# Performance work log

Hardware: AMD Instinct MI355X
Metric: run time of the kernel (lower is better)

The kernel has to match this reference:

```python
import jax, jax.numpy as jnp
import numpy as np

N_NODES = 100000


def setup_inputs() -> dict:
    key = jax.random.key(0)
    k1, k2, k3 = jax.random.split(key, 3)
    X = jax.random.normal(k1, (N_NODES, 128), dtype=jnp.float32)
    W = jax.random.normal(k2, (128, 128), dtype=jnp.float32) * (1.0 / np.sqrt(128))
    edge_index = jax.random.randint(k3, (2, 1600000), 0, N_NODES, dtype=jnp.int64)
    return {"X": X, "W": W, "edge_index": edge_index}


def reference(X, W, edge_index):
    # GCNConv: out = D_hat^{-1/2} (A + I) D_hat^{-1/2} @ (X W^T)
    N = X.shape[0]
    row, col = edge_index[0], edge_index[1]
    # A_hat = A + I : append self-loop edges
    loops = jnp.arange(N, dtype=row.dtype)
    row_h = jnp.concatenate([row, loops])
    col_h = jnp.concatenate([col, loops])
    # D_hat = A_hat.sum(0): column sums -> degree indexed by col
    deg = jax.ops.segment_sum(jnp.ones(col_h.shape[0], dtype=X.dtype), col_h,
                              num_segments=N)
    d_invsqrt = deg ** -0.5  # deg >= 1 due to self loops
    # edge value of H = D^-1/2 A_hat D^-1/2
    val = d_invsqrt[row_h] * d_invsqrt[col_h]  # [E+N]
    # linear projection (nn.Linear, no bias): X @ W^T
    X_hat = X @ W.T  # [N, out]
    # SpMM (sum): out[r] += val * X_hat[c]
    msgs = val[:, None] * X_hat[col_h]  # [E+N, out]
    return jax.ops.segment_sum(msgs, row_h, num_segments=N)
```

## Files before the change

kernel.cpp:

```cpp
#include <hip/hip_runtime.h>
#include <hip/hip_bf16.h>
#include <stdint.h>

typedef __bf16 bf16_t;
typedef bf16_t bf16x8 __attribute__((ext_vector_type(8)));
typedef bf16_t bf16x2 __attribute__((ext_vector_type(2)));
typedef float  f32x4  __attribute__((ext_vector_type(4)));
typedef float  f32x2  __attribute__((ext_vector_type(2)));

#define N_FEAT 128
#define NBMAX  196
#define BINB   512

__global__ void detect_k(const int* __restrict__ edges, int* __restrict__ flag) {
    int v = edges[2 * threadIdx.x + 1];
    unsigned long long m = __ballot(v != 0);
    if (threadIdx.x == 0) *flag = (m == 0ull) ? 1 : 0;
}
__device__ inline int eread(const int* __restrict__ edges, int f, long i) {
    return f ? edges[2 * i] : edges[i];
}

__device__ inline bf16x8 cvt8(const float* __restrict__ p) {
    f32x4 lo = *(const f32x4*)p;
    f32x4 hi = *(const f32x4*)(p + 4);
    bf16x8 r;
    r[0] = (bf16_t)lo[0]; r[1] = (bf16_t)lo[1]; r[2] = (bf16_t)lo[2]; r[3] = (bf16_t)lo[3];
    r[4] = (bf16_t)hi[0]; r[5] = (bf16_t)hi[1]; r[6] = (bf16_t)hi[2]; r[7] = (bf16_t)hi[3];
    return r;
}

__device__ inline int block_scan_incl(int v, int* wsum ) {
    const int t = threadIdx.x, lane = t & 63, wid = t >> 6;
    int x = v;
#pragma unroll
    for (int off = 1; off < 64; off <<= 1) {
        int y = __shfl_up(x, off);
        if (lane >= off) x += y;
    }
    if (lane == 63) wsum[wid] = x;
    __syncthreads();
    int add = 0;
    for (int w = 0; w < wid; ++w) add += wsum[w];
    return x + add;
}

__global__ __launch_bounds__(256) void wconv_k(const float* __restrict__ W,
                                               bf16_t* __restrict__ Wbf) {
    int i = blockIdx.x * 256 + threadIdx.x;
    Wbf[i] = (bf16_t)W[i];
}

__global__ __launch_bounds__(64) void gemm_xwt2(const float* __restrict__ X,
                                                const bf16_t* __restrict__ Wbf,
                                                bf16_t* __restrict__ Xhat) {
    const int lane = threadIdx.x;
    const int m  = lane & 15;
    const int kq = lane >> 4;
    const long r0 = (long)blockIdx.x * 16;

    f32x4 acc[8];
#pragma unroll
    for (int c = 0; c < 8; ++c) acc[c] = (f32x4){0.f, 0.f, 0.f, 0.f};

    const float* xrow = X + (r0 + m) * N_FEAT + kq * 8;
#pragma unroll
    for (int kb = 0; kb < 4; ++kb) {
        bf16x8 a = cvt8(xrow + kb * 32);
#pragma unroll
        for (int c = 0; c < 8; ++c) {
            bf16x8 b = *(const bf16x8*)(Wbf + (c * 16 + m) * N_FEAT + kb * 32 + kq * 8);
            acc[c] = __builtin_amdgcn_mfma_f32_16x16x32_bf16(a, b, acc[c], 0, 0, 0);
        }
    }
#pragma unroll
    for (int c = 0; c < 8; ++c) {
#pragma unroll
        for (int i = 0; i < 4; ++i) {
            long r = r0 + kq * 4 + i;
            Xhat[r * N_FEAT + c * 16 + m] = (bf16_t)acc[c][i];
        }
    }
}


__global__ __launch_bounds__(256) void bin_k(const int* __restrict__ edges,
                                             const int* __restrict__ flag,
                                             int E, int N, int NB,
                                             int* __restrict__ hist) {
    __shared__ int h[2 * NBMAX];
    const int blk = blockIdx.x;
    const int nb2 = 2 * NB;
    for (int j = threadIdx.x; j < nb2; j += 256) h[j] = 0;
    __syncthreads();
    const int f = *flag;
    const int chunk = (E + BINB - 1) / BINB;
    const int e0 = blk * chunk, e1 = min(E, e0 + chunk);
    if (f) {
        const int2* e2 = (const int2*)edges;
        for (int e = e0 + (int)threadIdx.x; e < e1; e += 256) {
            int r = e2[e].x, c = e2[(long)E + e].x;
            if ((unsigned)r < (unsigned)N && (unsigned)c < (unsigned)N) {
                atomicAdd(&h[r >> 9], 1);
                atomicAdd(&h[NB + (c >> 9)], 1);
            }
        }
    } else {
        for (int e = e0 + (int)threadIdx.x; e < e1; e += 256) {
            int r = edges[e], c = edges[(long)E + e];
            if ((unsigned)r < (unsigned)N && (unsigned)c < (unsigned)N) {
                atomicAdd(&h[r >> 9], 1);
                atomicAdd(&h[NB + (c >> 9)], 1);
            }
        }
    }
    __syncthreads();
    for (int j = threadIdx.x; j < nb2; j += 256) hist[(long)j * BINB + blk] = h[j];
}

__global__ __launch_bounds__(BINB) void scan_k(const int* __restrict__ hist, int NB,
                                               int* __restrict__ baseTab,
                                               int* __restrict__ totals) {
    __shared__ int wsum[BINB / 64];
    const int j = blockIdx.x;
    const int t = threadIdx.x;
    int v = hist[(long)j * BINB + t];
    int incl = block_scan_incl(v, wsum);
    baseTab[(long)j * BINB + t] = incl - v;
    if (t == BINB - 1) totals[j] = incl;
}

__global__ __launch_bounds__(512) void bucketbase_k(const int* __restrict__ totals,
                                                    int NB, int N,
                                                    int* __restrict__ famBase,
                                                    int* __restrict__ start) {
    __shared__ int wsum[8];
    __shared__ int sh_tot0;
    const int t = threadIdx.x;
    const int nb2 = 2 * NB;
    int v = (t < nb2) ? totals[t] : 0;
    int incl = block_scan_incl(v, wsum);
    int excl = incl - v;
    if (t == NB) sh_tot0 = excl;
    __syncthreads();
    if (t < NB) famBase[t] = excl;
    if (t == NB) { famBase[NB] = excl; start[N] = excl; }
    if (t >= NB && t < nb2) famBase[NB + 1 + (t - NB)] = excl - sh_tot0;
    if (t == nb2 - 1) famBase[NB + 1 + NB] = incl - sh_tot0;
}

__global__ __launch_bounds__(256) void bscatter_k(const int* __restrict__ edges,
                                                  const int* __restrict__ flag,
                                                  int E, int N, int NB,
                                                  const int* __restrict__ baseTab,
                                                  const int* __restrict__ famBase,
                                                  unsigned* __restrict__ rowbuf,
                                                  int* __restrict__ colbuf) {
    __shared__ int cur[2 * NBMAX];
    const int blk = blockIdx.x;
    const int nb2 = 2 * NB;
    for (int j = threadIdx.x; j < nb2; j += 256) {
        int fb = (j < NB) ? famBase[j] : famBase[NB + 1 + (j - NB)];
        cur[j] = fb + baseTab[(long)j * BINB + blk];
    }
    __syncthreads();
    const int f = *flag;
    const int chunk = (E + BINB - 1) / BINB;
    const int e0 = blk * chunk, e1 = min(E, e0 + chunk);
    if (f) {
        const int2* e2 = (const int2*)edges;
        for (int e = e0 + (int)threadIdx.x; e < e1; e += 256) {
            int r = e2[e].x, c = e2[(long)E + e].x;
            if ((unsigned)r < (unsigned)N && (unsigned)c < (unsigned)N) {
                int pr = atomicAdd(&cur[r >> 9], 1);
                rowbuf[pr] = ((unsigned)(r & 511) << 17) | (unsigned)c;
                int pc = atomicAdd(&cur[NB + (c >> 9)], 1);
                colbuf[pc] = c & 511;
            }
        }
    } else {
        for (int e = e0 + (int)threadIdx.x; e < e1; e += 256) {
            int r = edges[e], c = edges[(long)E + e];
            if ((unsigned)r < (unsigned)N && (unsigned)c < (unsigned)N) {
                int pr = atomicAdd(&cur[r >> 9], 1);
                rowbuf[pr] = ((unsigned)(r & 511) << 17) | (unsigned)c;
                int pc = atomicAdd(&cur[NB + (c >> 9)], 1);
                colbuf[pc] = c & 511;
            }
        }
    }
}

__global__ __launch_bounds__(512) void degcsr_k(const unsigned* __restrict__ rowbuf,
                                                const int* __restrict__ colbuf,
                                                const int* __restrict__ famBase,
                                                int NB, int N,
                                                int* __restrict__ start,
                                                int* __restrict__ ecol,
                                                float* __restrict__ dinv) {
    __shared__ int cnt[512];
    __shared__ int wsum[8];
    const int t = threadIdx.x;
    if ((int)blockIdx.x >= NB) {
        const int b = blockIdx.x - NB;
        cnt[t] = 0;
        __syncthreads();
        const int e0 = famBase[NB + 1 + b], e1 = famBase[NB + 1 + b + 1];
        for (int e = e0 + t; e < e1; e += 512)
            atomicAdd(&cnt[colbuf[e]], 1);
        __syncthreads();
        int n = (b << 9) + t;
        if (n < N) dinv[n] = rsqrtf((float)(cnt[t] + 1));
        return;
    }
    const int b = blockIdx.x;
    cnt[t] = 0;
    __syncthreads();
    const int e0 = famBase[b], e1 = famBase[b + 1];
    for (int e = e0 + t; e < e1; e += 512)
        atomicAdd(&cnt[rowbuf[e] >> 17], 1);
    __syncthreads();
    int v = cnt[t];
    int incl = block_scan_incl(v, wsum);
    int excl = incl - v;
    const int n = (b << 9) + t;
    if (n < N) start[n] = e0 + excl;
    cnt[t] = e0 + excl;
    __syncthreads();
    for (int e = e0 + t; e < e1; e += 512) {
        unsigned w = rowbuf[e];
        int pos = atomicAdd(&cnt[w >> 17], 1);
        ecol[pos] = (int)(w & 0x1FFFFu);
    }
}

__global__ __launch_bounds__(64) void gather3_k(const int* __restrict__ ecol,
                                                const int* __restrict__ start,
                                                const float* __restrict__ dinv,
                                                const bf16_t* __restrict__ Xhat,
                                                float* __restrict__ out) {
    const int n = blockIdx.x;
    const int j = threadIdx.x;
    const int s = start[n], e = start[n + 1];
    const float dn = dinv[n];

    bf16x2 xs = *(const bf16x2*)(Xhat + (long)n * N_FEAT + 2 * j);
    float a0 = dn * (float)xs[0];
    float a1 = dn * (float)xs[1];

    for (int p = s; p < e; p += 8) {
        int   cq[8];
        float dq[8];
#pragma unroll
        for (int q = 0; q < 8; ++q) {
            int tt = p + q;
            int idx = (tt < e) ? tt : s;
            cq[q] = ecol[idx];
            dq[q] = (tt < e) ? dinv[cq[q]] : 0.0f;
        }
#pragma unroll
        for (int q = 0; q < 8; ++q) {
            bf16x2 xv = *(const bf16x2*)(Xhat + (long)cq[q] * N_FEAT + 2 * j);
            a0 += dq[q] * (float)xv[0];
            a1 += dq[q] * (float)xv[1];
        }
    }
    f32x2 o; o[0] = dn * a0; o[1] = dn * a1;
    *(f32x2*)(out + (long)n * N_FEAT + 2 * j) = o;
}


__global__ __launch_bounds__(64) void gemm_xwt(const float* __restrict__ X,
                                               const float* __restrict__ W,
                                               bf16_t* __restrict__ Xhat) {
    const int lane = threadIdx.x;
    const int m  = lane & 15;
    const int kq = lane >> 4;
    const long r0 = (long)blockIdx.x * 16;
    f32x4 acc[8];
#pragma unroll
    for (int c = 0; c < 8; ++c) acc[c] = (f32x4){0.f, 0.f, 0.f, 0.f};
    const float* xrow = X + (r0 + m) * N_FEAT + kq * 8;
#pragma unroll
    for (int kb = 0; kb < 4; ++kb) {
        bf16x8 a = cvt8(xrow + kb * 32);
#pragma unroll
        for (int c = 0; c < 8; ++c) {
            bf16x8 b = cvt8(W + (c * 16 + m) * N_FEAT + kb * 32 + kq * 8);
            acc[c] = __builtin_amdgcn_mfma_f32_16x16x32_bf16(a, b, acc[c], 0, 0, 0);
        }
    }
#pragma unroll
    for (int c = 0; c < 8; ++c)
#pragma unroll
        for (int i = 0; i < 4; ++i) {
            long r = r0 + kq * 4 + i;
            Xhat[r * N_FEAT + c * 16 + m] = (bf16_t)acc[c][i];
        }
}

__global__ void degree_k(const int* __restrict__ edges, const int* __restrict__ flag,
                         int E, int N,
                         int* __restrict__ cnt_row, int* __restrict__ cnt_col) {
    int e = blockIdx.x * blockDim.x + threadIdx.x;
    int f = *flag;
    if (e < E) {
        int r = eread(edges, f, e);
        int c = eread(edges, f, (long)E + e);
        if ((unsigned)r < (unsigned)N) atomicAdd(&cnt_row[r], 1);
        if ((unsigned)c < (unsigned)N) atomicAdd(&cnt_col[c], 1);
    }
}

__global__ void degree_col_k(const int* __restrict__ edges, const int* __restrict__ flag,
                             int E, int N, int* __restrict__ cnt_col) {
    int e = blockIdx.x * blockDim.x + threadIdx.x;
    int f = *flag;
    if (e < E) {
        int c = eread(edges, f, (long)E + e);
        if ((unsigned)c < (unsigned)N) atomicAdd(&cnt_col[c], 1);
    }
}

__global__ void alloc_k(const int* __restrict__ cnt_row, int N,
                        int* __restrict__ cur, int* __restrict__ total,
                        int* cnt_col_in, float* dinv_out) {
    int n = blockIdx.x * blockDim.x + threadIdx.x;
    if (n < N) {
        cur[n] = atomicAdd(total, cnt_row[n]);
        int dc = cnt_col_in[n];
        dinv_out[n] = rsqrtf((float)(dc + 1));
    }
}

__global__ void scatter_k(const int* __restrict__ edges, const int* __restrict__ flag,
                          int E, int N, int* __restrict__ cur, int* __restrict__ ecol) {
    int e = blockIdx.x * blockDim.x + threadIdx.x;
    int f = *flag;
    if (e < E) {
        int r = eread(edges, f, e);
        if ((unsigned)r < (unsigned)N) {
            int p = atomicAdd(&cur[r], 1);
            if ((unsigned)p < (unsigned)E)
                ecol[p] = eread(edges, f, (long)E + e);
        }
    }
}

__global__ __launch_bounds__(64) void gather_k(const int* __restrict__ ecol,
                                               const int* __restrict__ cur,
                                               const int* __restrict__ cnt_row,
                                               const float* __restrict__ dinv,
                                               const bf16_t* __restrict__ Xhat,
                                               int N,
                                               float* __restrict__ out) {
    const int n = blockIdx.x;
    const int j = threadIdx.x;
    const int c = cnt_row[n];
    const int s = cur[n] - c;
    const float dn = dinv[n];
    bf16x2 xs = *(const bf16x2*)(Xhat + (long)n * N_FEAT + 2 * j);
    float a0 = dn * (float)xs[0];
    float a1 = dn * (float)xs[1];
    for (int e = 0; e < c; ++e) {
        int cc = ecol[s + e];
        if ((unsigned)cc >= (unsigned)N) continue;
        float dc = dinv[cc];
        bf16x2 xv = *(const bf16x2*)(Xhat + (long)cc * N_FEAT + 2 * j);
        a0 += dc * (float)xv[0];
        a1 += dc * (float)xv[1];
    }
    f32x2 o; o[0] = dn * a0; o[1] = dn * a1;
    *(f32x2*)(out + (long)n * N_FEAT + 2 * j) = o;
}


__global__ __launch_bounds__(128) void self_k(const int* __restrict__ cnt_col,
                                              const bf16_t* __restrict__ Xhat,
                                              float* __restrict__ out) {
    const int n = blockIdx.x;
    const int j = threadIdx.x;
    const float dn2 = 1.0f / (float)(cnt_col[n] + 1);
    out[(long)n * N_FEAT + j] = dn2 * (float)Xhat[(long)n * N_FEAT + j];
}

__global__ __launch_bounds__(128) void edge_add_k(const int* __restrict__ edges,
                                                  const int* __restrict__ flag,
                                                  int E, int N,
                                                  const int* __restrict__ cnt_col,
                                                  const bf16_t* __restrict__ Xhat,
                                                  float* __restrict__ out) {
    const int e = blockIdx.x;
    const int j = threadIdx.x;
    int f = *flag;
    const int r = eread(edges, f, e);
    const int c = eread(edges, f, (long)E + e);
    if ((unsigned)r >= (unsigned)N || (unsigned)c >= (unsigned)N) return;
    const float val = rsqrtf((float)(cnt_col[r] + 1)) * rsqrtf((float)(cnt_col[c] + 1));
    atomicAdd(&out[(long)r * N_FEAT + j], val * (float)Xhat[(long)c * N_FEAT + j]);
}

extern "C" void kernel_launch(void* const* d_in, const int* in_sizes, int n_in,
                              void* d_out, int out_size, void* d_ws, size_t ws_size,
                              hipStream_t stream) {
    const float* X = (const float*)d_in[0];
    const float* W = (const float*)d_in[1];
    const int* edges = (const int*)d_in[2];
    const int E = in_sizes[2] / 2;
    const int N = in_sizes[0] / N_FEAT;
    const int NB = (N + 511) >> 9;

    char* ws = (char*)d_ws;
    const size_t xhat_b = (size_t)N * N_FEAT * sizeof(bf16_t);
    const size_t n4     = (size_t)N * 4;
    auto al = [](size_t x) { return (x + 255) & ~(size_t)255; };

    size_t off = 0;
    int*      flag   = (int*)(ws + off);        off = 256;
    bf16_t*   Wbf    = (bf16_t*)(ws + off);     off = al(off + 128 * 128 * 2);
    bf16_t*   Xhat   = (bf16_t*)(ws + off);     off = al(off + xhat_b);
    float*    dinv   = (float*)(ws + off);      off = al(off + n4);
    int*      startA = (int*)(ws + off);        off = al(off + n4 + 4);
    unsigned* rowbuf = (unsigned*)(ws + off);   off = al(off + (size_t)E * 4);
    int*      colbuf = (int*)(ws + off);        off = al(off + (size_t)E * 4);
    int*      ecol   = (int*)(ws + off);        off = al(off + (size_t)E * 4);
    int*      hist   = (int*)(ws + off);        off = al(off + (size_t)BINB * 2 * NB * 4);
    int*      baseTab= (int*)(ws + off);        off = al(off + (size_t)BINB * 2 * NB * 4);
    int*      totals = (int*)(ws + off);        off = al(off + (size_t)(2 * NB) * 4);
    int*      famBase= (int*)(ws + off);        off = al(off + (size_t)(2 * NB + 2) * 4);
    const size_t need_S = off;

    int* cnt_col = (int*)(ws + 16 + xhat_b);
    const size_t need_A = 16 + xhat_b + n4 * 3 + 16 + (size_t)E * 4;
    const size_t need_B = 16 + xhat_b + n4;

    if (ws_size >= need_S && NB <= NBMAX && N <= 100352 && (N & 15) == 0 && E >= BINB) {
        detect_k<<<1, 64, 0, stream>>>(edges, flag);
        wconv_k<<<64, 256, 0, stream>>>(W, Wbf);
        gemm_xwt2<<<N / 16, 64, 0, stream>>>(X, Wbf, Xhat);
        bin_k<<<BINB, 256, 0, stream>>>(edges, flag, E, N, NB, hist);
        scan_k<<<2 * NB, BINB, 0, stream>>>(hist, NB, baseTab, totals);
        bucketbase_k<<<1, 512, 0, stream>>>(totals, NB, N, famBase, startA);
        bscatter_k<<<BINB, 256, 0, stream>>>(edges, flag, E, N, NB, baseTab, famBase,
                                             rowbuf, colbuf);
        degcsr_k<<<2 * NB, 512, 0, stream>>>(rowbuf, colbuf, famBase, NB, N,
                                             startA, ecol, dinv);
        gather3_k<<<N, 64, 0, stream>>>(ecol, startA, dinv, Xhat, (float*)d_out);
    } else if (ws_size >= need_A) {
        bf16_t* XhatA  = (bf16_t*)(ws + 16);
        int*   cnt_row = (int*)(ws + 16 + xhat_b + n4);
        int*   cur     = (int*)(ws + 16 + xhat_b + n4 * 2);
        int*   total   = (int*)(ws + 16 + xhat_b + n4 * 3);
        int*   ecolA   = (int*)(ws + 16 + xhat_b + n4 * 3 + 16);
        float* dinvA   = (float*)cnt_col;

        hipMemsetAsync(cnt_col, 0, n4 * 2, stream);
        hipMemsetAsync(total, 0, 16, stream);
        detect_k<<<1, 64, 0, stream>>>(edges, flag);
        gemm_xwt<<<N / 16, 64, 0, stream>>>(X, W, XhatA);
        degree_k<<<(E + 255) / 256, 256, 0, stream>>>(edges, flag, E, N, cnt_row, cnt_col);
        alloc_k<<<(N + 255) / 256, 256, 0, stream>>>(cnt_row, N, cur, total, cnt_col, dinvA);
        scatter_k<<<(E + 255) / 256, 256, 0, stream>>>(edges, flag, E, N, cur, ecolA);
        gather_k<<<N, 64, 0, stream>>>(ecolA, cur, cnt_row, dinvA, XhatA, N, (float*)d_out);
    } else if (ws_size >= need_B) {
        bf16_t* XhatB = (bf16_t*)(ws + 16);
        hipMemsetAsync(cnt_col, 0, n4, stream);
        detect_k<<<1, 64, 0, stream>>>(edges, flag);
        gemm_xwt<<<N / 16, 64, 0, stream>>>(X, W, XhatB);
        degree_col_k<<<(E + 255) / 256, 256, 0, stream>>>(edges, flag, E, N, cnt_col);
        self_k<<<N, 128, 0, stream>>>(cnt_col, XhatB, (float*)d_out);
        edge_add_k<<<E, 128, 0, stream>>>(edges, flag, E, N, cnt_col, XhatB, (float*)d_out);
    }
}
```

Before: 270.8 us.

## Prescale Xhat by dinv in GEMM and drop per-edge dinv gathers

The GEMM now runs after the degree computation and multiplies each output row by its inverse-sqrt degree before writing bf16 Xhat. The gather therefore skips the per-edge dinv lookup, sending padded lanes to a zero row appended to Xhat instead. The separate detect kernel is folded into bin_k and bscatter_k, which removes one launch. The cost is that the GEMM can no longer overlap the graph-build kernels in stream order, and pre-scaling before the bf16 rounding changes numerics slightly.

Measured after the change: 242.5 us. 10.5% less time.

```diff
diff --git a/kernel.cpp b/kernel.cpp
--- a/kernel.cpp
+++ b/kernel.cpp
@@ -19,6 +19,16 @@
 }
 __device__ inline int eread(const int* __restrict__ edges, int f, long i) {
     return f ? edges[2 * i] : edges[i];
+}
+
+__device__ inline int detect_inline(const int* __restrict__ edges, int* sh) {
+    if (threadIdx.x < 64) {
+        int v = edges[2 * threadIdx.x + 1];
+        unsigned long long m = __ballot(v != 0);
+        if (threadIdx.x == 0) sh[0] = (m == 0ull) ? 1 : 0;
+    }
+    __syncthreads();
+    return sh[0];
 }
 
 __device__ inline bf16x8 cvt8(const float* __restrict__ p) {
@@ -46,13 +56,19 @@
 }
 
 __global__ __launch_bounds__(256) void wconv_k(const float* __restrict__ W,
-                                               bf16_t* __restrict__ Wbf) {
-    int i = blockIdx.x * 256 + threadIdx.x;
-    Wbf[i] = (bf16_t)W[i];
-}
-
-__global__ __launch_bounds__(64) void gemm_xwt2(const float* __restrict__ X,
+                                               bf16_t* __restrict__ Wbf,
+                                               bf16_t* __restrict__ xpad) {
+    if (blockIdx.x < 64) {
+        int i = blockIdx.x * 256 + threadIdx.x;
+        Wbf[i] = (bf16_t)W[i];
+    } else if (threadIdx.x < N_FEAT) {
+        xpad[threadIdx.x] = (bf16_t)0.0f;
+    }
+}
+
+__global__ __launch_bounds__(64) void gemm_xwts(const float* __restrict__ X,
                                                 const bf16_t* __restrict__ Wbf,
+                                                const float* __restrict__ dinv,
                                                 bf16_t* __restrict__ Xhat) {
     const int lane = threadIdx.x;
     const int m  = lane & 15;
@@ -73,27 +89,30 @@
             acc[c] = __builtin_amdgcn_mfma_f32_16x16x32_bf16(a, b, acc[c], 0, 0, 0);
         }
     }
+    float dr[4];
+#pragma unroll
+    for (int i = 0; i < 4; ++i) dr[i] = dinv[r0 + kq * 4 + i];
 #pragma unroll
     for (int c = 0; c < 8; ++c) {
 #pragma unroll
         for (int i = 0; i < 4; ++i) {
             long r = r0 + kq * 4 + i;
-            Xhat[r * N_FEAT + c * 16 + m] = (bf16_t)acc[c][i];
+            Xhat[r * N_FEAT + c * 16 + m] = (bf16_t)(dr[i] * acc[c][i]);
         }
     }
 }
 
 
 __global__ __launch_bounds__(256) void bin_k(const int* __restrict__ edges,
-                                             const int* __restrict__ flag,
                                              int E, int N, int NB,
                                              int* __restrict__ hist) {
     __shared__ int h[2 * NBMAX];
+    __shared__ int shf[1];
+    const int f = detect_inline(edges, shf);
     const int blk = blockIdx.x;
     const int nb2 = 2 * NB;
     for (int j = threadIdx.x; j < nb2; j += 256) h[j] = 0;
     __syncthreads();
-    const int f = *flag;
     const int chunk = (E + BINB - 1) / BINB;
     const int e0 = blk * chunk, e1 = min(E, e0 + chunk);
     if (f) {
@@ -150,13 +169,14 @@
 }
 
 __global__ __launch_bounds__(256) void bscatter_k(const int* __restrict__ edges,
-                                                  const int* __restrict__ flag,
                                                   int E, int N, int NB,
                                                   const int* __restrict__ baseTab,
                                                   const int* __restrict__ famBase,
                                                   unsigned* __restrict__ rowbuf,
                                                   int* __restrict__ colbuf) {
     __shared__ int cur[2 * NBMAX];
+    __shared__ int shf[1];
+    const int f = detect_inline(edges, shf);
     const int blk = blockIdx.x;
     const int nb2 = 2 * NB;
     for (int j = threadIdx.x; j < nb2; j += 256) {
@@ -164,7 +184,6 @@
         cur[j] = fb + baseTab[(long)j * BINB + blk];
     }
     __syncthreads();
-    const int f = *flag;
     const int chunk = (E + BINB - 1) / BINB;
     const int e0 = blk * chunk, e1 = min(E, e0 + chunk);
     if (f) {
@@ -234,37 +253,37 @@
     }
 }
 
-__global__ __launch_bounds__(64) void gather3_k(const int* __restrict__ ecol,
+__global__ __launch_bounds__(64) void gather5_k(const int* __restrict__ ecol,
                                                 const int* __restrict__ start,
                                                 const float* __restrict__ dinv,
                                                 const bf16_t* __restrict__ Xhat,
+                                                int N,
                                                 float* __restrict__ out) {
     const int n = blockIdx.x;
     const int j = threadIdx.x;
     const int s = start[n], e = start[n + 1];
-    const float dn = dinv[n];
 
     bf16x2 xs = *(const bf16x2*)(Xhat + (long)n * N_FEAT + 2 * j);
-    float a0 = dn * (float)xs[0];
-    float a1 = dn * (float)xs[1];
+    float a0 = (float)xs[0];
+    float a1 = (float)xs[1];
 
     for (int p = s; p < e; p += 8) {
-        int   cq[8];
-        float dq[8];
+        int cq[8];
 #pragma unroll
         for (int q = 0; q < 8; ++q) {
             int tt = p + q;
             int idx = (tt < e) ? tt : s;
-            cq[q] = ecol[idx];
-            dq[q] = (tt < e) ? dinv[cq[q]] : 0.0f;
+            int cc = ecol[idx];
+            cq[q] = (tt < e) ? cc : N;
         }
 #pragma unroll
         for (int q = 0; q < 8; ++q) {
             bf16x2 xv = *(const bf16x2*)(Xhat + (long)cq[q] * N_FEAT + 2 * j);
-            a0 += dq[q] * (float)xv[0];
-            a1 += dq[q] * (float)xv[1];
-        }
-    }
+            a0 += (float)xv[0];
+            a1 += (float)xv[1];
+        }
+    }
+    const float dn = dinv[n];
     f32x2 o; o[0] = dn * a0; o[1] = dn * a1;
     *(f32x2*)(out + (long)n * N_FEAT + 2 * j) = o;
 }
@@ -411,7 +430,7 @@
     const int NB = (N + 511) >> 9;
 
     char* ws = (char*)d_ws;
-    const size_t xhat_b = (size_t)N * N_FEAT * sizeof(bf16_t);
+    const size_t xhat_b = (size_t)(N + 1) * N_FEAT * sizeof(bf16_t);
     const size_t n4     = (size_t)N * 4;
     auto al = [](size_t x) { return (x + 255) & ~(size_t)255; };
 
@@ -435,17 +454,16 @@
     const size_t need_B = 16 + xhat_b + n4;
 
     if (ws_size >= need_S && NB <= NBMAX && N <= 100352 && (N & 15) == 0 && E >= BINB) {
-        detect_k<<<1, 64, 0, stream>>>(edges, flag);
-        wconv_k<<<64, 256, 0, stream>>>(W, Wbf);
-        gemm_xwt2<<<N / 16, 64, 0, stream>>>(X, Wbf, Xhat);
-        bin_k<<<BINB, 256, 0, stream>>>(edges, flag, E, N, NB, hist);
+        wconv_k<<<65, 256, 0, stream>>>(W, Wbf, Xhat + (size_t)N * N_FEAT);
+        bin_k<<<BINB, 256, 0, stream>>>(edges, E, N, NB, hist);
         scan_k<<<2 * NB, BINB, 0, stream>>>(hist, NB, baseTab, totals);
         bucketbase_k<<<1, 512, 0, stream>>>(totals, NB, N, famBase, startA);
-        bscatter_k<<<BINB, 256, 0, stream>>>(edges, flag, E, N, NB, baseTab, famBase,
+        bscatter_k<<<BINB, 256, 0, stream>>>(edges, E, N, NB, baseTab, famBase,
                                              rowbuf, colbuf);
         degcsr_k<<<2 * NB, 512, 0, stream>>>(rowbuf, colbuf, famBase, NB, N,
                                              startA, ecol, dinv);
-        gather3_k<<<N, 64, 0, stream>>>(ecol, startA, dinv, Xhat, (float*)d_out);
+        gemm_xwts<<<N / 16, 64, 0, stream>>>(X, Wbf, dinv, Xhat);
+        gather5_k<<<N, 64, 0, stream>>>(ecol, startA, dinv, Xhat, N, (float*)d_out);
     } else if (ws_size >= need_A) {
         bf16_t* XhatA  = (bf16_t*)(ws + 16);
         int*   cnt_row = (int*)(ws + 16 + xhat_b + n4);
```
